# Performance work log

Hardware: AMD Instinct MI355X
Metric: run time of the kernel (lower is better)

The kernel has to match this reference:

```python
import jax, jax.numpy as jnp
import numpy as np


def setup_inputs() -> dict:
    key = jax.random.key(0)
    ks = jax.random.split(key, 5)
    B, S, D = 2, 2048, 1024
    std = 0.02
    return {
        "x": jax.random.normal(ks[0], (B, S, D), dtype=jnp.float32),
        "Wq": jax.random.normal(ks[1], (D, D), dtype=jnp.float32) * std,
        "Wk": jax.random.normal(ks[2], (D, D), dtype=jnp.float32) * std,
        "Wv": jax.random.normal(ks[3], (D, D), dtype=jnp.float32) * std,
        "Wo": jax.random.normal(ks[4], (D, D), dtype=jnp.float32) * std,
        "num_heads": 16,
        "window_size": 512,
    }


def reference(x, Wq, Wk, Wv, Wo, num_heads, window_size):
    B, S, D = x.shape
    H = num_heads
    d = D // H
    scale = d ** (-0.5)

    # QKV projections (torch Linear: y = x @ W.T), split heads -> b h s d
    def proj(W):
        return (x @ W.T).reshape(B, S, H, d).transpose(0, 2, 1, 3)

    q, k, v = proj(Wq), proj(Wk), proj(Wv)

    # [B, H, S, S] scores (faithful to the dense SDPA fallback)
    scores = jnp.einsum("bhsd,bhtd->bhst", q, k) * scale

    # sliding-window causal mask: col <= row and row - col < window_size
    pos = jnp.arange(S)
    row, col = pos[:, None], pos[None, :]
    mask = (col <= row) & (row - col < window_size)  # [S, S]
    scores = jnp.where(mask[None, None], scores, -jnp.inf)

    attn = jax.nn.softmax(scores, axis=-1)
    out = jnp.einsum("bhst,bhtd->bhsd", attn, v)  # b h s d
    out = out.transpose(0, 2, 1, 3).reshape(B, S, D)  # merge heads
    return out @ Wo.T
```

## Files before the change

### kernel.cpp

```cpp
#include <hip/hip_runtime.h>
#include <cstdint>

typedef uint16_t u16;
typedef __attribute__((ext_vector_type(8))) short short8;
typedef __attribute__((ext_vector_type(4))) float f32x4;

__device__ __forceinline__ u16 f2bf(float f) {
  uint32_t u = __float_as_uint(f);
  u += 0x7fff + ((u >> 16) & 1);
  return (u16)(u >> 16);
}
__device__ __forceinline__ uint32_t pk2bf(float a, float b) {
  uint32_t ua = __float_as_uint(a) + 0x8000u;
  uint32_t ub = __float_as_uint(b) + 0x8000u;
  return (ua >> 16) | (ub & 0xFFFF0000u);
}

#define GLL16(gp, lp) __builtin_amdgcn_global_load_lds( \
    (__attribute__((address_space(1))) void*)(gp), \
    (__attribute__((address_space(3))) void*)(lp), 16, 0, 0)

#define SBAR()       __builtin_amdgcn_s_barrier()
#define WAIT_LGKM0() asm volatile("s_waitcnt lgkmcnt(0)" ::: "memory")
#define WAIT_VM(N)   asm volatile("s_waitcnt vmcnt(" #N ")" ::: "memory")
#define MEMBAR()     asm volatile("" ::: "memory")

template<int N> __device__ __forceinline__ void wait_vm() {
  static_assert(N == 0 || N == 4 || N == 6 || N == 8 || N == 10 || N == 12, "add literal case");
  if constexpr (N == 0)  { WAIT_VM(0); }
  else if constexpr (N == 4)  { WAIT_VM(4); }
  else if constexpr (N == 6)  { WAIT_VM(6); }
  else if constexpr (N == 8)  { WAIT_VM(8); }
  else if constexpr (N == 10) { WAIT_VM(10); }
  else if constexpr (N == 12) { WAIT_VM(12); }
}

__global__ void cvt_all(const float* __restrict__ x,  const float* __restrict__ wq,
                        const float* __restrict__ wk, const float* __restrict__ wv,
                        const float* __restrict__ wo,
                        u16* __restrict__ xb, u16* __restrict__ wcat, u16* __restrict__ wob) {
  int i = blockIdx.x * 256 + threadIdx.x;
  const float4* src; ushort4* dst; int off; float sc = 1.0f;
  if (i < 1048576)      { src = (const float4*)x;  dst = (ushort4*)xb;              off = i; }
  else if (i < 1310720) { src = (const float4*)wq; dst = (ushort4*)wcat;            off = i - 1048576;
                          sc = 0.18033688011112042f; }
  else if (i < 1572864) { src = (const float4*)wk; dst = (ushort4*)wcat + 262144;   off = i - 1310720; }
  else if (i < 1835008) { src = (const float4*)wv; dst = (ushort4*)wcat + 524288;   off = i - 1572864; }
  else                  { src = (const float4*)wo; dst = (ushort4*)wob;             off = i - 1835008; }
  float4 v = src[off];
  ushort4 o;
  o.x = f2bf(v.x * sc); o.y = f2bf(v.y * sc); o.z = f2bf(v.z * sc); o.w = f2bf(v.w * sc);
  dst[off] = o;
}

template<int BM, int BN, int OUT_BF16>
__global__ __launch_bounds__(256, 2) void gemm_t(const u16* __restrict__ A,
                                                 const u16* __restrict__ B,
                                                 void* __restrict__ Cout,
                                                 int N, int K, int ntN) {
  constexpr int MF = BM / 32;
  constexpr int NF = BN / 32;
  constexpr int G  = (BM + BN) / 32;
  __shared__ u16 smA[2][BM * 64];
  __shared__ u16 smB[2][BN * 64];
  const int tid  = threadIdx.x;
  const int lane = tid & 63, w = tid >> 6;
  const int wr = w >> 1, wc = w & 1;
  const int g = lane >> 4, lr = lane & 15;

  const int cpx = gridDim.x >> 3;
  const int id  = blockIdx.x;
  const int sw  = (id & 7) * cpx + (id >> 3);
  const int row0 = (sw / ntN) * BM, col0 = (sw % ntN) * BN;
  const int T = K >> 6;

  f32x4 acc[MF][NF];
  #pragma unroll
  for (int i = 0; i < MF; ++i)
    #pragma unroll
    for (int j = 0; j < NF; ++j) acc[i][j] = (f32x4){0.f, 0.f, 0.f, 0.f};

  auto STAGE = [&](int kt, int bufi) {
    #pragma unroll
    for (int j = 0; j < BM / 32; ++j) {
      int r  = j * 32 + w * 8 + (lane >> 3);
      int sb = ((lane & 7) << 4) ^ ((r & 7) << 4);
      GLL16(A + (size_t)(row0 + r) * K + kt * 64 + (sb >> 1),
            &smA[bufi][(size_t)(j * 32 + w * 8) * 64]);
    }
    #pragma unroll
    for (int j = 0; j < BN / 32; ++j) {
      int r  = j * 32 + w * 8 + (lane >> 3);
      int sb = ((lane & 7) << 4) ^ ((r & 7) << 4);
      GLL16(B + (size_t)(col0 + r) * K + kt * 64 + (sb >> 1),
            &smB[bufi][(size_t)(j * 32 + w * 8) * 64]);
    }
  };

  STAGE(0, 0); STAGE(1, 1);
  wait_vm<G>(); SBAR(); MEMBAR();

  for (int t = 0; t < T; ++t) {
    const int cur = t & 1;
    short8 a[MF][2], b[NF][2];
    #pragma unroll
    for (int mm = 0; mm < MF; ++mm)
      #pragma unroll
      for (int kh = 0; kh < 2; ++kh) {
        int row = wr * (BM / 2) + mm * 16 + lr;
        int col = (kh * 64 + g * 16) ^ ((row & 7) << 4);
        a[mm][kh] = *(const short8*)((const char*)&smA[cur][0] + row * 128 + col);
      }
    #pragma unroll
    for (int nn = 0; nn < NF; ++nn)
      #pragma unroll
      for (int kh = 0; kh < 2; ++kh) {
        int row = wc * (BN / 2) + nn * 16 + lr;
        int col = (kh * 64 + g * 16) ^ ((row & 7) << 4);
        b[nn][kh] = *(const short8*)((const char*)&smB[cur][0] + row * 128 + col);
      }
    WAIT_LGKM0(); MEMBAR(); SBAR(); MEMBAR();

    if (t + 2 < T) STAGE(t + 2, cur);

    __builtin_amdgcn_s_setprio(1);
    #pragma unroll
    for (int kh = 0; kh < 2; ++kh)
      #pragma unroll
      for (int mm = 0; mm < MF; ++mm)
        #pragma unroll
        for (int nn = 0; nn < NF; ++nn)
          acc[mm][nn] = __builtin_amdgcn_mfma_f32_16x16x32_bf16(
              a[mm][kh], b[nn][kh], acc[mm][nn], 0, 0, 0);
    __builtin_amdgcn_s_setprio(0);

    if (t + 1 < T) {
      if (t + 2 < T) { wait_vm<G>(); } else { wait_vm<0>(); }
      SBAR(); MEMBAR();
    }
  }

  #pragma unroll
  for (int i = 0; i < MF; ++i)
    #pragma unroll
    for (int j = 0; j < NF; ++j)
      #pragma unroll
      for (int ri = 0; ri < 4; ++ri) {
        int rr = row0 + wr * (BM / 2) + i * 16 + g * 4 + ri;
        int cc = col0 + wc * (BN / 2) + j * 16 + lr;
        if (OUT_BF16) ((u16*)Cout)[(size_t)rr * N + cc] = f2bf(acc[i][j][ri]);
        else          ((float*)Cout)[(size_t)rr * N + cc] = acc[i][j][ri];
      }
}

__global__ __launch_bounds__(256, 3) void attn_swa(const u16* __restrict__ QKV, u16* __restrict__ O) {
  const int S = 2048;
  const int qb = blockIdx.x * 128;
  const int b = blockIdx.y >> 4, h = blockIdx.y & 15;
  const int tid = threadIdx.x;
  const int lane = tid & 63, w = tid >> 6;
  const int g = lane >> 4, lr = lane & 15;

  __shared__ u16 Klds[2][64 * 64];
  __shared__ u16 Vt[2][64][72];
  __shared__ u16 Plds[4][32][72];

  const u16* Qb = QKV + (size_t)b * S * 3072 + h * 64;
  const u16* Kb = QKV + (size_t)b * S * 3072 + 1024 + h * 64;
  const u16* Vb = QKV + (size_t)b * S * 3072 + 2048 + h * 64;

  const int qw = qb + w * 32;
  short8 qf[2][2];
  #pragma unroll
  for (int qg = 0; qg < 2; ++qg)
    #pragma unroll
    for (int kh = 0; kh < 2; ++kh)
      qf[qg][kh] = *(const short8*)(Qb + (size_t)(qw + qg * 16 + lr) * 3072 + kh * 32 + g * 8);

  float ls[2] = {0.f, 0.f};
  f32x4 accO[2][4];
  #pragma unroll
  for (int qg = 0; qg < 2; ++qg)
    #pragma unroll
    for (int i = 0; i < 4; ++i) accO[qg][i] = (f32x4){0.f, 0.f, 0.f, 0.f};

  int ks = qb - 511; if (ks < 0) ks = 0; ks &= ~63;
  const int ke = qb + 127;
  const int nt = ((ke - ks) >> 6) + 1;

  short8 vreg0, vreg1;

  auto STAGE_K = [&](int kb, int buf) {
    #pragma unroll
    for (int c = 0; c < 2; ++c) {
      int r  = c * 32 + w * 8 + (lane >> 3);
      int sb = ((lane & 7) << 4) ^ ((r & 7) << 4);
      const u16* gp = Kb + (size_t)(kb + r) * 3072 + (sb >> 1);
      u16* lp = Klds[buf] + c * 2048 + w * 512;
      GLL16(gp, lp);
    }
  };
  auto LOAD_V = [&](int kb) {
    vreg0 = *(const short8*)(Vb + (size_t)(kb + lane) * 3072 + w * 8);
    vreg1 = *(const short8*)(Vb + (size_t)(kb + lane) * 3072 + w * 8 + 32);
  };
  auto WRITE_V = [&](int buf) {
    #pragma unroll
    for (int j = 0; j < 8; ++j) Vt[buf][w * 8 + j][lane]      = (u16)vreg0[j];
    #pragma unroll
    for (int j = 0; j < 8; ++j) Vt[buf][w * 8 + 32 + j][lane] = (u16)vreg1[j];
  };

  LOAD_V(ks); MEMBAR();
  STAGE_K(ks, 0); MEMBAR();
  WAIT_VM(0); MEMBAR();
  SBAR(); MEMBAR();
  WRITE_V(0);

  int cur = 0, kb = ks;
  for (int t = 0; t < nt; ++t, kb += 64) {
    const int nxt = cur ^ 1;
    const bool more = (t + 1 < nt);
    if (more) { LOAD_V(kb + 64); MEMBAR(); STAGE_K(kb + 64, nxt); MEMBAR(); }

    const bool active = (kb <= qw + 31) && (kb + 63 >= qw - 511);
    if (active) {
      float p[2][4][4];
      #pragma unroll
      for (int st = 0; st < 4; ++st) {
        f32x4 c4[2];
        c4[0] = (f32x4){0.f, 0.f, 0.f, 0.f};
        c4[1] = (f32x4){0.f, 0.f, 0.f, 0.f};
        int r = st * 16 + lr;
        int swz = (r & 7) << 4;
        const char* krow = (const char*)(Klds[cur]) + r * 128;
        short8 kf0 = *(const short8*)(krow + ((g * 16) ^ swz));
        short8 kf1 = *(const short8*)(krow + ((64 + g * 16) ^ swz));
        __builtin_amdgcn_s_setprio(1);
        c4[0] = __builtin_amdgcn_mfma_f32_16x16x32_bf16(kf0, qf[0][0], c4[0], 0, 0, 0);
        c4[1] = __builtin_amdgcn_mfma_f32_16x16x32_bf16(kf0, qf[1][0], c4[1], 0, 0, 0);
        c4[0] = __builtin_amdgcn_mfma_f32_16x16x32_bf16(kf1, qf[0][1], c4[0], 0, 0, 0);
        c4[1] = __builtin_amdgcn_mfma_f32_16x16x32_bf16(kf1, qf[1][1], c4[1], 0, 0, 0);
        __builtin_amdgcn_s_setprio(0);
        #pragma unroll
        for (int ri = 0; ri < 4; ++ri) { p[0][st][ri] = c4[0][ri]; p[1][st][ri] = c4[1][ri]; }
      }

      #pragma unroll
      for (int qg = 0; qg < 2; ++qg) {
        const int q0 = qw + qg * 16;
        const bool clean = (kb + 63 <= q0) && (q0 + 15 - kb < 512);
        if (clean) {
          #pragma unroll
          for (int st = 0; st < 4; ++st)
            #pragma unroll
            for (int ri = 0; ri < 4; ++ri)
              p[qg][st][ri] = __builtin_amdgcn_exp2f(p[qg][st][ri]);
        } else {
          const int base = q0 + lr - kb;
          #pragma unroll
          for (int st = 0; st < 4; ++st)
            #pragma unroll
            for (int ri = 0; ri < 4; ++ri) {
              float e = __builtin_amdgcn_exp2f(p[qg][st][ri]);
              p[qg][st][ri] = ((uint32_t)(base - (st * 16 + g * 4 + ri)) < 512u) ? e : 0.f;
            }
        }
        float s = 0.f;
        #pragma unroll
        for (int st = 0; st < 4; ++st)
          #pragma unroll
          for (int ri = 0; ri < 4; ++ri) s += p[qg][st][ri];
        s += __shfl_xor(s, 16);
        s += __shfl_xor(s, 32);
        ls[qg] += s;

        #pragma unroll
        for (int st = 0; st < 4; ++st) {
          uint2 u2;
          u2.x = pk2bf(p[qg][st][0], p[qg][st][1]);
          u2.y = pk2bf(p[qg][st][2], p[qg][st][3]);
          *(uint2*)(&Plds[w][qg * 16 + lr][st * 16 + g * 4]) = u2;
        }
      }
    }

    if (more) { WAIT_VM(0); MEMBAR(); }
    WAIT_LGKM0(); MEMBAR();
    SBAR(); MEMBAR();
    if (more) WRITE_V(nxt);

    if (active) {
      short8 pf[2][2];
      #pragma unroll
      for (int qg = 0; qg < 2; ++qg) {
        pf[qg][0] = *(const short8*)(&Plds[w][qg * 16 + lr][g * 8]);
        pf[qg][1] = *(const short8*)(&Plds[w][qg * 16 + lr][32 + g * 8]);
      }
      __builtin_amdgcn_s_setprio(1);
      #pragma unroll
      for (int dt = 0; dt < 4; ++dt) {
        short8 vf0 = *(const short8*)(&Vt[cur][dt * 16 + lr][g * 8]);
        short8 vf1 = *(const short8*)(&Vt[cur][dt * 16 + lr][32 + g * 8]);
        accO[0][dt] = __builtin_amdgcn_mfma_f32_16x16x32_bf16(pf[0][0], vf0, accO[0][dt], 0, 0, 0);
        accO[1][dt] = __builtin_amdgcn_mfma_f32_16x16x32_bf16(pf[1][0], vf0, accO[1][dt], 0, 0, 0);
        accO[0][dt] = __builtin_amdgcn_mfma_f32_16x16x32_bf16(pf[0][1], vf1, accO[0][dt], 0, 0, 0);
        accO[1][dt] = __builtin_amdgcn_mfma_f32_16x16x32_bf16(pf[1][1], vf1, accO[1][dt], 0, 0, 0);
      }
      __builtin_amdgcn_s_setprio(0);
    }
    cur = nxt;
  }

  #pragma unroll
  for (int qg = 0; qg < 2; ++qg) {
    float lsq[4];
    #pragma unroll
    for (int ri = 0; ri < 4; ++ri) lsq[ri] = __shfl(ls[qg], g * 4 + ri);
    #pragma unroll
    for (int dt = 0; dt < 4; ++dt)
      #pragma unroll
      for (int ri = 0; ri < 4; ++ri) {
        int qi = qw + qg * 16 + g * 4 + ri;
        O[(size_t)(b * S + qi) * 1024 + h * 64 + dt * 16 + lr] = f2bf(accO[qg][dt][ri] / lsq[ri]);
      }
  }
}

extern "C" void kernel_launch(void* const* d_in, const int* in_sizes, int n_in,
                              void* d_out, int out_size, void* d_ws, size_t ws_size,
                              hipStream_t stream) {
  const float* x  = (const float*)d_in[0];
  const float* Wq = (const float*)d_in[1];
  const float* Wk = (const float*)d_in[2];
  const float* Wv = (const float*)d_in[3];
  const float* Wo = (const float*)d_in[4];

  char* ws = (char*)d_ws;
  u16* xb   = (u16*)(ws);
  u16* Wcat = (u16*)(ws + (8  << 20));
  u16* Wob  = (u16*)(ws + (14 << 20));
  u16* QKV  = (u16*)(ws + (16 << 20));
  u16* Oatt = (u16*)(ws + (40 << 20));

  cvt_all<<<8192, 256, 0, stream>>>(x, Wq, Wk, Wv, Wo, xb, Wcat, Wob);
  gemm_t<128, 192, 1><<<512, 256, 0, stream>>>(xb, Wcat, QKV, 3072, 1024, 16);
  attn_swa<<<dim3(16, 32), 256, 0, stream>>>(QKV, Oatt);
  gemm_t<64, 128, 0><<<512, 256, 0, stream>>>(Oatt, Wob, d_out, 1024, 1024, 8);
}
```

Before: 83.83 us.

## Split attention block across 8 waves with 16 query rows each

```diff
diff --git a/kernel.cpp b/kernel.cpp
--- a/kernel.cpp
+++ b/kernel.cpp
@@ -153,7 +153,7 @@
       }
 }
 
-__global__ __launch_bounds__(256, 3) void attn_swa(const u16* __restrict__ QKV, u16* __restrict__ O) {
+__global__ __launch_bounds__(512, 4) void attn_swa(const u16* __restrict__ QKV, u16* __restrict__ O) {
   const int S = 2048;
   const int qb = blockIdx.x * 128;
   const int b = blockIdx.y >> 4, h = blockIdx.y & 15;
@@ -163,52 +163,42 @@
 
   __shared__ u16 Klds[2][64 * 64];
   __shared__ u16 Vt[2][64][72];
-  __shared__ u16 Plds[4][32][72];
+  __shared__ u16 Plds[8][16][72];
 
   const u16* Qb = QKV + (size_t)b * S * 3072 + h * 64;
   const u16* Kb = QKV + (size_t)b * S * 3072 + 1024 + h * 64;
   const u16* Vb = QKV + (size_t)b * S * 3072 + 2048 + h * 64;
 
-  const int qw = qb + w * 32;
-  short8 qf[2][2];
-  #pragma unroll
-  for (int qg = 0; qg < 2; ++qg)
-    #pragma unroll
-    for (int kh = 0; kh < 2; ++kh)
-      qf[qg][kh] = *(const short8*)(Qb + (size_t)(qw + qg * 16 + lr) * 3072 + kh * 32 + g * 8);
-
-  float ls[2] = {0.f, 0.f};
-  f32x4 accO[2][4];
-  #pragma unroll
-  for (int qg = 0; qg < 2; ++qg)
-    #pragma unroll
-    for (int i = 0; i < 4; ++i) accO[qg][i] = (f32x4){0.f, 0.f, 0.f, 0.f};
+  const int qw = qb + w * 16;
+  short8 qf[2];
+  #pragma unroll
+  for (int kh = 0; kh < 2; ++kh)
+    qf[kh] = *(const short8*)(Qb + (size_t)(qw + lr) * 3072 + kh * 32 + g * 8);
+
+  float ls = 0.f;
+  f32x4 accO[4];
+  #pragma unroll
+  for (int i = 0; i < 4; ++i) accO[i] = (f32x4){0.f, 0.f, 0.f, 0.f};
 
   int ks = qb - 511; if (ks < 0) ks = 0; ks &= ~63;
   const int ke = qb + 127;
   const int nt = ((ke - ks) >> 6) + 1;
 
-  short8 vreg0, vreg1;
+  short8 vreg;
 
   auto STAGE_K = [&](int kb, int buf) {
-    #pragma unroll
-    for (int c = 0; c < 2; ++c) {
-      int r  = c * 32 + w * 8 + (lane >> 3);
-      int sb = ((lane & 7) << 4) ^ ((r & 7) << 4);
-      const u16* gp = Kb + (size_t)(kb + r) * 3072 + (sb >> 1);
-      u16* lp = Klds[buf] + c * 2048 + w * 512;
-      GLL16(gp, lp);
-    }
+    int r  = w * 8 + (lane >> 3);
+    int sb = ((lane & 7) << 4) ^ ((r & 7) << 4);
+    const u16* gp = Kb + (size_t)(kb + r) * 3072 + (sb >> 1);
+    u16* lp = Klds[buf] + w * 512;
+    GLL16(gp, lp);
   };
   auto LOAD_V = [&](int kb) {
-    vreg0 = *(const short8*)(Vb + (size_t)(kb + lane) * 3072 + w * 8);
-    vreg1 = *(const short8*)(Vb + (size_t)(kb + lane) * 3072 + w * 8 + 32);
+    vreg = *(const short8*)(Vb + (size_t)(kb + lane) * 3072 + w * 8);
   };
   auto WRITE_V = [&](int buf) {
     #pragma unroll
-    for (int j = 0; j < 8; ++j) Vt[buf][w * 8 + j][lane]      = (u16)vreg0[j];
-    #pragma unroll
-    for (int j = 0; j < 8; ++j) Vt[buf][w * 8 + 32 + j][lane] = (u16)vreg1[j];
+    for (int j = 0; j < 8; ++j) Vt[buf][w * 8 + j][lane] = (u16)vreg[j];
   };
 
   LOAD_V(ks); MEMBAR();
@@ -223,65 +213,58 @@
     const bool more = (t + 1 < nt);
     if (more) { LOAD_V(kb + 64); MEMBAR(); STAGE_K(kb + 64, nxt); MEMBAR(); }
 
-    const bool active = (kb <= qw + 31) && (kb + 63 >= qw - 511);
+    const bool active = (kb <= qw + 15) && (kb + 63 >= qw - 511);
     if (active) {
-      float p[2][4][4];
+      float p[4][4];
       #pragma unroll
       for (int st = 0; st < 4; ++st) {
-        f32x4 c4[2];
-        c4[0] = (f32x4){0.f, 0.f, 0.f, 0.f};
-        c4[1] = (f32x4){0.f, 0.f, 0.f, 0.f};
+        f32x4 c4 = (f32x4){0.f, 0.f, 0.f, 0.f};
         int r = st * 16 + lr;
         int swz = (r & 7) << 4;
         const char* krow = (const char*)(Klds[cur]) + r * 128;
         short8 kf0 = *(const short8*)(krow + ((g * 16) ^ swz));
         short8 kf1 = *(const short8*)(krow + ((64 + g * 16) ^ swz));
         __builtin_amdgcn_s_setprio(1);
-        c4[0] = __builtin_amdgcn_mfma_f32_16x16x32_bf16(kf0, qf[0][0], c4[0], 0, 0, 0);
-        c4[1] = __builtin_amdgcn_mfma_f32_16x16x32_bf16(kf0, qf[1][0], c4[1], 0, 0, 0);
-        c4[0] = __builtin_amdgcn_mfma_f32_16x16x32_bf16(kf1, qf[0][1], c4[0], 0, 0, 0);
-        c4[1] = __builtin_amdgcn_mfma_f32_16x16x32_bf16(kf1, qf[1][1], c4[1], 0, 0, 0);
+        c4 = __builtin_amdgcn_mfma_f32_16x16x32_bf16(kf0, qf[0], c4, 0, 0, 0);
+        c4 = __builtin_amdgcn_mfma_f32_16x16x32_bf16(kf1, qf[1], c4, 0, 0, 0);
         __builtin_amdgcn_s_setprio(0);
         #pragma unroll
-        for (int ri = 0; ri < 4; ++ri) { p[0][st][ri] = c4[0][ri]; p[1][st][ri] = c4[1][ri]; }
-      }
-
-      #pragma unroll
-      for (int qg = 0; qg < 2; ++qg) {
-        const int q0 = qw + qg * 16;
-        const bool clean = (kb + 63 <= q0) && (q0 + 15 - kb < 512);
-        if (clean) {
-          #pragma unroll
-          for (int st = 0; st < 4; ++st)
-            #pragma unroll
-            for (int ri = 0; ri < 4; ++ri)
-              p[qg][st][ri] = __builtin_amdgcn_exp2f(p[qg][st][ri]);
-        } else {
-          const int base = q0 + lr - kb;
-          #pragma unroll
-          for (int st = 0; st < 4; ++st)
-            #pragma unroll
-            for (int ri = 0; ri < 4; ++ri) {
-              float e = __builtin_amdgcn_exp2f(p[qg][st][ri]);
-              p[qg][st][ri] = ((uint32_t)(base - (st * 16 + g * 4 + ri)) < 512u) ? e : 0.f;
-            }
-        }
-        float s = 0.f;
+        for (int ri = 0; ri < 4; ++ri) p[st][ri] = c4[ri];
+      }
+
+      const bool clean = (kb + 63 <= qw) && (qw + 15 - kb < 512);
+      if (clean) {
         #pragma unroll
         for (int st = 0; st < 4; ++st)
           #pragma unroll
-          for (int ri = 0; ri < 4; ++ri) s += p[qg][st][ri];
+          for (int ri = 0; ri < 4; ++ri)
+            p[st][ri] = __builtin_amdgcn_exp2f(p[st][ri]);
+      } else {
+        const int base = qw + lr - kb;
+        #pragma unroll
+        for (int st = 0; st < 4; ++st)
+          #pragma unroll
+          for (int ri = 0; ri < 4; ++ri) {
+            float e = __builtin_amdgcn_exp2f(p[st][ri]);
+            p[st][ri] = ((uint32_t)(base - (st * 16 + g * 4 + ri)) < 512u) ? e : 0.f;
+          }
+      }
+      {
+        float s = 0.f;
+        #pragma unroll
+        for (int st = 0; st < 4; ++st)
+          #pragma unroll
+          for (int ri = 0; ri < 4; ++ri) s += p[st][ri];
         s += __shfl_xor(s, 16);
         s += __shfl_xor(s, 32);
-        ls[qg] += s;
-
-        #pragma unroll
-        for (int st = 0; st < 4; ++st) {
-          uint2 u2;
-          u2.x = pk2bf(p[qg][st][0], p[qg][st][1]);
-          u2.y = pk2bf(p[qg][st][2], p[qg][st][3]);
-          *(uint2*)(&Plds[w][qg * 16 + lr][st * 16 + g * 4]) = u2;
-        }
+        ls += s;
+      }
+      #pragma unroll
+      for (int st = 0; st < 4; ++st) {
+        uint2 u2;
+        u2.x = pk2bf(p[st][0], p[st][1]);
+        u2.y = pk2bf(p[st][2], p[st][3]);
+        *(uint2*)(&Plds[w][lr][st * 16 + g * 4]) = u2;
       }
     }
 
@@ -291,40 +274,31 @@
     if (more) WRITE_V(nxt);
 
     if (active) {
-      short8 pf[2][2];
-      #pragma unroll
-      for (int qg = 0; qg < 2; ++qg) {
-        pf[qg][0] = *(const short8*)(&Plds[w][qg * 16 + lr][g * 8]);
-        pf[qg][1] = *(const short8*)(&Plds[w][qg * 16 + lr][32 + g * 8]);
-      }
+      short8 pf0 = *(const short8*)(&Plds[w][lr][g * 8]);
+      short8 pf1 = *(const short8*)(&Plds[w][lr][32 + g * 8]);
       __builtin_amdgcn_s_setprio(1);
       #pragma unroll
       for (int dt = 0; dt < 4; ++dt) {
         short8 vf0 = *(const short8*)(&Vt[cur][dt * 16 + lr][g * 8]);
         short8 vf1 = *(const short8*)(&Vt[cur][dt * 16 + lr][32 + g * 8]);
-        accO[0][dt] = __builtin_amdgcn_mfma_f32_16x16x32_bf16(pf[0][0], vf0, accO[0][dt], 0, 0, 0);
-        accO[1][dt] = __builtin_amdgcn_mfma_f32_16x16x32_bf16(pf[1][0], vf0, accO[1][dt], 0, 0, 0);
-        accO[0][dt] = __builtin_amdgcn_mfma_f32_16x16x32_bf16(pf[0][1], vf1, accO[0][dt], 0, 0, 0);
-        accO[1][dt] = __builtin_amdgcn_mfma_f32_16x16x32_bf16(pf[1][1], vf1, accO[1][dt], 0, 0, 0);
+        accO[dt] = __builtin_amdgcn_mfma_f32_16x16x32_bf16(pf0, vf0, accO[dt], 0, 0, 0);
+        accO[dt] = __builtin_amdgcn_mfma_f32_16x16x32_bf16(pf1, vf1, accO[dt], 0, 0, 0);
       }
       __builtin_amdgcn_s_setprio(0);
     }
     cur = nxt;
   }
 
-  #pragma unroll
-  for (int qg = 0; qg < 2; ++qg) {
-    float lsq[4];
-    #pragma unroll
-    for (int ri = 0; ri < 4; ++ri) lsq[ri] = __shfl(ls[qg], g * 4 + ri);
-    #pragma unroll
-    for (int dt = 0; dt < 4; ++dt)
-      #pragma unroll
-      for (int ri = 0; ri < 4; ++ri) {
-        int qi = qw + qg * 16 + g * 4 + ri;
-        O[(size_t)(b * S + qi) * 1024 + h * 64 + dt * 16 + lr] = f2bf(accO[qg][dt][ri] / lsq[ri]);
-      }
-  }
+  float lsq[4];
+  #pragma unroll
+  for (int ri = 0; ri < 4; ++ri) lsq[ri] = __shfl(ls, g * 4 + ri);
+  #pragma unroll
+  for (int dt = 0; dt < 4; ++dt)
+    #pragma unroll
+    for (int ri = 0; ri < 4; ++ri) {
+      int qi = qw + g * 4 + ri;
+      O[(size_t)(b * S + qi) * 1024 + h * 64 + dt * 16 + lr] = f2bf(accO[dt][ri] / lsq[ri]);
+    }
 }
 
 extern "C" void kernel_launch(void* const* d_in, const int* in_sizes, int n_in,
@@ -345,6 +319,6 @@
 
   cvt_all<<<8192, 256, 0, stream>>>(x, Wq, Wk, Wv, Wo, xb, Wcat, Wob);
   gemm_t<128, 192, 1><<<512, 256, 0, stream>>>(xb, Wcat, QKV, 3072, 1024, 16);
-  attn_swa<<<dim3(16, 32), 256, 0, stream>>>(QKV, Oatt);
+  attn_swa<<<dim3(16, 32), 512, 0, stream>>>(QKV, Oatt);
   gemm_t<64, 128, 0><<<512, 256, 0, stream>>>(Oatt, Wob, d_out, 1024, 1024, 8);
 }
```

Result: no change. 82.57 us (-1.5%).
